# Kernel optimization log

Hardware: AMD Instinct MI355X
Metric: run time of the kernel (lower is better)

Reference implementation:

```python
import jax, jax.numpy as jnp
import numpy as np

PAD = 0          # pad_token_id == blank_index in the source module
NEG = -1e30      # log-space 'zero' (safe for fp32)


def _ctc_mean_loss(labels, logits, logits_mask):
    """Faithful jnp port of CTCLoss.call: tf.nn.ctc_loss (alpha forward DP,
    blank=pad, dense labels, logits [B,T,V]) + feasibility mask + mean."""
    B, T, V = logits.shape
    L = labels.shape[1]
    S = 2 * L + 1

    labels_len = jnp.sum(labels != PAD, axis=-1).astype(jnp.int32)   # [B]
    logits_len = jnp.sum(logits_mask, axis=-1).astype(jnp.int32)     # [B]

    logp = jax.nn.log_softmax(logits.astype(jnp.float32), axis=-1)   # [B,T,V]

    # Blank-interleaved extended label sequence: (blank, l1, blank, l2, ..., blank)
    ext = jnp.full((B, S), PAD, dtype=labels.dtype)
    ext = ext.at[:, 1::2].set(labels)                                # [B,S]
    ext_m2 = jnp.pad(ext, ((0, 0), (2, 0)), constant_values=PAD)[:, :S]
    allow_skip = (ext != PAD) & (ext != ext_m2)                      # [B,S]

    # Emission log-probs gathered at extended labels: em[b,t,s] = logp[b,t,ext[b,s]]
    em = jnp.take_along_axis(logp, jnp.broadcast_to(ext[:, None, :], (B, T, S)), axis=2)
    em = em.transpose(1, 0, 2)                                       # [T,B,S]

    neg = jnp.float32(NEG)
    alpha0 = jnp.full((B, S), neg, dtype=jnp.float32)
    alpha0 = alpha0.at[:, 0].set(em[0, :, 0]).at[:, 1].set(em[0, :, 1])

    t_idx = jnp.arange(1, T, dtype=jnp.int32)
    active = t_idx[:, None] < logits_len[None, :]                    # [T-1,B]

    def step(alpha, inp):
        em_t, act = inp                                              # [B,S], [B]
        p1 = jnp.concatenate([jnp.full((B, 1), neg), alpha[:, :-1]], axis=1)
        p2 = jnp.concatenate([jnp.full((B, 2), neg), alpha[:, :-2]], axis=1)
        p2 = jnp.where(allow_skip, p2, neg)
        new = em_t + jnp.logaddexp(jnp.logaddexp(alpha, p1), p2)
        alpha = jnp.where(act[:, None], new, alpha)                  # freeze past logit_len
        return alpha, None

    alpha, _ = jax.lax.scan(step, alpha0, (em[1:], active))          # [B,S]

    e = 2 * labels_len                                               # end of extended seq
    a_end = jnp.take_along_axis(alpha, e[:, None], axis=1)[:, 0]
    a_end1 = jnp.take_along_axis(alpha, jnp.maximum(e - 1, 0)[:, None], axis=1)[:, 0]
    loss = -jnp.logaddexp(a_end, a_end1)                             # per-example NLL

    loss_mask = (labels_len <= logits_len).astype(jnp.float32)
    return jnp.mean(loss * loss_mask)


def setup_inputs() -> dict:
    key = jax.random.key(0)
    k1, k2, k3, k4 = jax.random.split(key, 4)
    B, T, V, L = 256, 1024, 64, 64

    lab_len = jax.random.randint(k1, (B,), L // 2, L + 1)            # [32,64]
    vals = jax.random.randint(k2, (B, L), 1, V)                      # non-blank tokens
    labels = jnp.where(jnp.arange(L)[None, :] < lab_len[:, None], vals, 0).astype(jnp.int64)

    log_len = jax.random.randint(k3, (B,), 2 * L + 64, T + 1)        # feasible alignments
    logits_mask = jnp.arange(T)[None, :] < log_len[:, None]          # prefix-True mask

    logits = jax.random.normal(k4, (B, T, V), dtype=jnp.float32)
    return {"labels": labels, "logits": logits, "logits_mask": logits_mask}


def reference(labels, logits, logits_mask):
    return _ctc_mean_loss(labels, logits, logits_mask)
```

## Files before the change

### kernel.cpp

```cpp
#include <hip/hip_runtime.h>

#define BB 256
#define TT 1024
#define VV 64
#define LL 64
#define LOG2E 1.4426950408889634f
#define LN2   0.6931471805599453f

__device__ __forceinline__ int   f2i(float x) { return __float_as_int(x); }
__device__ __forceinline__ float i2f(int x)   { return __int_as_float(x); }

__device__ __forceinline__ float wave_max63(float x) {
  x = fmaxf(x, i2f(__builtin_amdgcn_update_dpp(0, f2i(x), 0x111, 0xF, 0xF, true)));
  x = fmaxf(x, i2f(__builtin_amdgcn_update_dpp(0, f2i(x), 0x112, 0xF, 0xF, true)));
  x = fmaxf(x, i2f(__builtin_amdgcn_update_dpp(0, f2i(x), 0x114, 0xF, 0xF, true)));
  x = fmaxf(x, i2f(__builtin_amdgcn_update_dpp(0, f2i(x), 0x118, 0xF, 0xF, true)));
  x = fmaxf(x, i2f(__builtin_amdgcn_update_dpp(0, f2i(x), 0x142, 0xF, 0xF, true)));
  x = fmaxf(x, i2f(__builtin_amdgcn_update_dpp(0, f2i(x), 0x143, 0xF, 0xF, true)));
  return i2f(__builtin_amdgcn_readlane(f2i(x), 63));
}

extern "C" __global__ void __launch_bounds__(384, 1)
ctc_fused(const int* __restrict__ labels, const float* __restrict__ logits,
          const int* __restrict__ mask, float* __restrict__ out) {
  __shared__ float lsePart[4];
  __shared__ float sG0v[64], sG1v[64];
  __shared__ float sG2s;
  __shared__ int   sCtB;
  const int b = blockIdx.x;
  const int tid = threadIdx.x;
  const int lane = tid & 63;
  const int wv = tid >> 6;

  const float* lg = logits + (size_t)b * TT * VV;

  int lsum = 0;
  const int* mrow = mask + b * TT;
#pragma unroll
  for (int k = 0; k < TT / 64; ++k) lsum += mrow[lane + (k << 6)];
#pragma unroll
  for (int off = 32; off; off >>= 1) lsum += __shfl_xor(lsum, off);
  int len = __builtin_amdgcn_readfirstlane(lsum);
  len = len < 1 ? 1 : (len > TT ? TT : len);
  const int nwin = (len + 15) >> 4;
  int mid = len >> 1; mid = mid < 1 ? 1 : mid;
  const int nwF = (mid + 15) >> 4;
  const int nwB = (len - mid + 15) >> 4;

  int lab_len = 0;
  float A0 = 0.0f, A1 = 0.0f, A2 = 0.0f;
  int ctotA = 0;

#define RENORM3(X, Y, Z, CT) { \
    const float mxv = wave_max63(fmaxf(fmaxf(X, Y), Z)); \
    const int eb_ = (f2i(mxv) >> 23) & 255; \
    int kk = (eb_ > 0 && eb_ < 255) ? (187 - eb_) : 0; \
    kk = kk > 126 ? 126 : (kk < -126 ? -126 : kk); \
    CT += kk; \
    const float sc = i2f((127 + kk) << 23); \
    X *= sc; Y *= sc; Z *= sc; \
  }

#define RESCALE45(X, Y, Z, CT) { \
    const float mxv = wave_max63(fmaxf(fmaxf(X, Y), Z)); \
    const int eb_ = (f2i(mxv) >> 23) & 255; \
    int kk = (eb_ > 0 && eb_ < 255) ? (172 - eb_) : 0; \
    kk = kk > 126 ? 126 : (kk < -126 ? -126 : kk); \
    CT += kk; \
    const float sc = i2f((127 + kk) << 23); \
    X *= sc; Y *= sc; Z *= sc; \
  }

  if (wv == 0) {
    const int lab = labels[b * LL + lane] & 63;
    lab_len = (int)__popcll(__ballot(lab != 0));
    const int plab = __builtin_amdgcn_update_dpp(0, lab, 0x138, 0xF, 0xF, false);
    const float sk = (lab != 0 && lab != plab) ? 1.0f : 0.0f;
    A0 = (lane == 0) ? 1.0f : 0.0f;
    __builtin_amdgcn_s_setprio(1);

    const int cu = lane & 15;
    const float* lgg = lg + lab;
    const float* lgc = lg + (cu << 6);

    float qa_c, qb_c, qc_c;
    float qa_g0, qa_g1, qa_g2, qa_g3, qa_g4, qa_g5, qa_g6, qa_g7,
          qa_g8, qa_g9, qa_g10, qa_g11, qa_g12, qa_g13, qa_g14, qa_g15;
    float qb_g0, qb_g1, qb_g2, qb_g3, qb_g4, qb_g5, qb_g6, qb_g7,
          qb_g8, qb_g9, qb_g10, qb_g11, qb_g12, qb_g13, qb_g14, qb_g15;
    float qc_g0, qc_g1, qc_g2, qc_g3, qc_g4, qc_g5, qc_g6, qc_g7,
          qc_g8, qc_g9, qc_g10, qc_g11, qc_g12, qc_g13, qc_g14, qc_g15;

#define FISSUE(WN, S) { \
    const float* pg_ = lgg + ((WN) << 10); \
    S##_g0  = pg_[0];    S##_g1  = pg_[64];   S##_g2  = pg_[128];  S##_g3  = pg_[192]; \
    S##_g4  = pg_[256];  S##_g5  = pg_[320];  S##_g6  = pg_[384];  S##_g7  = pg_[448]; \
    S##_g8  = pg_[512];  S##_g9  = pg_[576];  S##_g10 = pg_[640];  S##_g11 = pg_[704]; \
    S##_g12 = pg_[768];  S##_g13 = pg_[832];  S##_g14 = pg_[896];  S##_g15 = pg_[960]; \
    S##_c = lgc[(WN) << 10]; \
  }

#define FSTEPU(U) { \
    const float A1p = i2f(__builtin_amdgcn_update_dpp(0, f2i(A1), 0x138, 0xF, 0xF, false)); \
    const float nA0 = c##U * (A0 + A1p); \
    const float nA1 = g##U * fmaf(sk, A1p, A0 + A1); \
    A2 = c##U * (A2 + A1); \
    A0 = nA0; A1 = nA1; \
  }

#define FSTEPM(U) { \
    const float A1p = i2f(__builtin_amdgcn_update_dpp(0, f2i(A1), 0x138, 0xF, 0xF, false)); \
    const float nA0 = c##U * (A0 + A1p); \
    const float nA1 = g##U * fmaf(sk, A1p, A0 + A1); \
    const float nA2 = c##U * (A2 + A1); \
    const bool act = (tbase + (U)) < mid; \
    A0 = act ? nA0 : A0; A1 = act ? nA1 : A1; A2 = act ? nA2 : A2; \
  }

#define FBODY(W, S) { \
    const float cv = __builtin_amdgcn_exp2f(S##_c * LOG2E); \
    const float g0  = __builtin_amdgcn_exp2f(S##_g0  * LOG2E); \
    const float g1  = __builtin_amdgcn_exp2f(S##_g1  * LOG2E); \
    const float g2  = __builtin_amdgcn_exp2f(S##_g2  * LOG2E); \
    const float g3  = __builtin_amdgcn_exp2f(S##_g3  * LOG2E); \
    const float g4  = __builtin_amdgcn_exp2f(S##_g4  * LOG2E); \
    const float g5  = __builtin_amdgcn_exp2f(S##_g5  * LOG2E); \
    const float g6  = __builtin_amdgcn_exp2f(S##_g6  * LOG2E); \
    const float g7  = __builtin_amdgcn_exp2f(S##_g7  * LOG2E); \
    const float g8  = __builtin_amdgcn_exp2f(S##_g8  * LOG2E); \
    const float g9  = __builtin_amdgcn_exp2f(S##_g9  * LOG2E); \
    const float g10 = __builtin_amdgcn_exp2f(S##_g10 * LOG2E); \
    const float g11 = __builtin_amdgcn_exp2f(S##_g11 * LOG2E); \
    const float g12 = __builtin_amdgcn_exp2f(S##_g12 * LOG2E); \
    const float g13 = __builtin_amdgcn_exp2f(S##_g13 * LOG2E); \
    const float g14 = __builtin_amdgcn_exp2f(S##_g14 * LOG2E); \
    const float g15 = __builtin_amdgcn_exp2f(S##_g15 * LOG2E); \
    if ((W) + 3 < 64) { FISSUE((W) + 3, S) } \
    const float c0  = i2f(__builtin_amdgcn_readlane(f2i(cv), 0)); \
    const float c1  = i2f(__builtin_amdgcn_readlane(f2i(cv), 1)); \
    const float c2  = i2f(__builtin_amdgcn_readlane(f2i(cv), 2)); \
    const float c3  = i2f(__builtin_amdgcn_readlane(f2i(cv), 3)); \
    const float c4  = i2f(__builtin_amdgcn_readlane(f2i(cv), 4)); \
    const float c5  = i2f(__builtin_amdgcn_readlane(f2i(cv), 5)); \
    const float c6  = i2f(__builtin_amdgcn_readlane(f2i(cv), 6)); \
    const float c7  = i2f(__builtin_amdgcn_readlane(f2i(cv), 7)); \
    const float c8  = i2f(__builtin_amdgcn_readlane(f2i(cv), 8)); \
    const float c9  = i2f(__builtin_amdgcn_readlane(f2i(cv), 9)); \
    const float c10 = i2f(__builtin_amdgcn_readlane(f2i(cv), 10)); \
    const float c11 = i2f(__builtin_amdgcn_readlane(f2i(cv), 11)); \
    const float c12 = i2f(__builtin_amdgcn_readlane(f2i(cv), 12)); \
    const float c13 = i2f(__builtin_amdgcn_readlane(f2i(cv), 13)); \
    const float c14 = i2f(__builtin_amdgcn_readlane(f2i(cv), 14)); \
    const float c15 = i2f(__builtin_amdgcn_readlane(f2i(cv), 15)); \
    RENORM3(A0, A1, A2, ctotA) \
    const int tbase = (W) << 4; \
    if (tbase + 16 <= mid) { \
      FSTEPU(0)  FSTEPU(1)  FSTEPU(2)  FSTEPU(3)  FSTEPU(4)  FSTEPU(5)  FSTEPU(6)  FSTEPU(7) \
      FSTEPU(8)  FSTEPU(9)  FSTEPU(10) FSTEPU(11) FSTEPU(12) FSTEPU(13) FSTEPU(14) FSTEPU(15) \
    } else { \
      FSTEPM(0)  FSTEPM(1)  FSTEPM(2)  FSTEPM(3)  FSTEPM(4)  FSTEPM(5)  FSTEPM(6)  FSTEPM(7) \
      FSTEPM(8)  FSTEPM(9)  FSTEPM(10) FSTEPM(11) FSTEPM(12) FSTEPM(13) FSTEPM(14) FSTEPM(15) \
    } \
  }

    FISSUE(0, qa) FISSUE(1, qb) FISSUE(2, qc)
    int w = 0;
    for (; w + 3 <= nwF; w += 3) {
      FBODY(w, qa) FBODY(w + 1, qb) FBODY(w + 2, qc)
    }
    if (w < nwF) { FBODY(w, qa) ++w; }
    if (w < nwF) { FBODY(w, qb) ++w; }
#undef FBODY
#undef FSTEPM
#undef FSTEPU
#undef FISSUE
    RESCALE45(A0, A1, A2, ctotA)

  } else if (wv == 1) {
    const int lab = labels[b * LL + lane] & 63;
    const int ll = (int)__popcll(__ballot(lab != 0));
    const int plab = __builtin_amdgcn_update_dpp(0, lab, 0x138, 0xF, 0xF, false);
    const float sk = (lab != 0 && lab != plab) ? 1.0f : 0.0f;
    const float skp = i2f(__builtin_amdgcn_update_dpp(0, f2i(sk), 0x130, 0xF, 0xF, false));
    const bool is63 = (lane == 63);
    __builtin_amdgcn_s_setprio(1);

    float G0 = 0.0f, G1 = 0.0f, G2 = 0.0f;
    if (ll == 0)            { G0 = (lane == 0) ? 2.0f : 0.0f; }
    else if (ll >= LL)      { G2 = 1.0f; G1 = is63 ? 1.0f : 0.0f; }
    else {
      G0 = (lane == ll) ? 1.0f : 0.0f;
      G1 = (lane == ll - 1) ? 1.0f : 0.0f;
    }
    int ctotB = 0;

    const int cu = lane & 15;
    const float* lgg = lg + lab;

    float ra_c, rb_c, rc_c;
    float ra_g0, ra_g1, ra_g2, ra_g3, ra_g4, ra_g5, ra_g6, ra_g7,
          ra_g8, ra_g9, ra_g10, ra_g11, ra_g12, ra_g13, ra_g14, ra_g15;
    float rb_g0, rb_g1, rb_g2, rb_g3, rb_g4, rb_g5, rb_g6, rb_g7,
          rb_g8, rb_g9, rb_g10, rb_g11, rb_g12, rb_g13, rb_g14, rb_g15;
    float rc_g0, rc_g1, rc_g2, rc_g3, rc_g4, rc_g5, rc_g6, rc_g7,
          rc_g8, rc_g9, rc_g10, rc_g11, rc_g12, rc_g13, rc_g14, rc_g15;

#define BLD(RW) ( (RW) < 0 ? 0 : (RW) )
#define BISSUE(J, S) { \
    const int br_ = len - 1 - ((J) << 4); \
    S##_g0  = lgg[BLD(br_ - 0)  << 6]; S##_g1  = lgg[BLD(br_ - 1)  << 6]; \
    S##_g2  = lgg[BLD(br_ - 2)  << 6]; S##_g3  = lgg[BLD(br_ - 3)  << 6]; \
    S##_g4  = lgg[BLD(br_ - 4)  << 6]; S##_g5  = lgg[BLD(br_ - 5)  << 6]; \
    S##_g6  = lgg[BLD(br_ - 6)  << 6]; S##_g7  = lgg[BLD(br_ - 7)  << 6]; \
    S##_g8  = lgg[BLD(br_ - 8)  << 6]; S##_g9  = lgg[BLD(br_ - 9)  << 6]; \
    S##_g10 = lgg[BLD(br_ - 10) << 6]; S##_g11 = lgg[BLD(br_ - 11) << 6]; \
    S##_g12 = lgg[BLD(br_ - 12) << 6]; S##_g13 = lgg[BLD(br_ - 13) << 6]; \
    S##_g14 = lgg[BLD(br_ - 14) << 6]; S##_g15 = lgg[BLD(br_ - 15) << 6]; \
    S##_c = lg[BLD(br_ - cu) << 6]; \
  }

#define BSTEPU(U) { \
    const float V_ = i2f(__builtin_amdgcn_update_dpp(0, f2i(G1), 0x130, 0xF, 0xF, false)); \
    float U_ = i2f(__builtin_amdgcn_update_dpp(0, f2i(G0), 0x130, 0xF, 0xF, false)); \
    U_ = is63 ? G2 : U_; \
    const float nG0 = fmaf(cB##U, G0, gB##U * G1); \
    const float nG1 = fmaf(gB##U, G1, fmaf(cB##U, U_, hB##U * V_)); \
    G2 = cB##U * G2; \
    G0 = nG0; G1 = nG1; \
  }

#define BSTEPM(U) { \
    const float V_ = i2f(__builtin_amdgcn_update_dpp(0, f2i(G1), 0x130, 0xF, 0xF, false)); \
    float U_ = i2f(__builtin_amdgcn_update_dpp(0, f2i(G0), 0x130, 0xF, 0xF, false)); \
    U_ = is63 ? G2 : U_; \
    const float nG0 = fmaf(cB##U, G0, gB##U * G1); \
    const float nG1 = fmaf(gB##U, G1, fmaf(cB##U, U_, hB##U * V_)); \
    const float nG2 = cB##U * G2; \
    const bool act = (brow0 - (U)) >= mid; \
    G0 = act ? nG0 : G0; G1 = act ? nG1 : G1; G2 = act ? nG2 : G2; \
  }

#define BPREP(U, S) \
    const float gB##U = __builtin_amdgcn_exp2f(S##_g##U * LOG2E); \
    const float hB##U = skp * i2f(__builtin_amdgcn_update_dpp(0, f2i(gB##U), 0x130, 0xF, 0xF, false));

#define BBODY(J, S) { \
    const int brow0 = len - 1 - ((J) << 4); \
    const float cv = __builtin_amdgcn_exp2f(S##_c * LOG2E); \
    BPREP(0, S)  BPREP(1, S)  BPREP(2, S)  BPREP(3, S) \
    BPREP(4, S)  BPREP(5, S)  BPREP(6, S)  BPREP(7, S) \
    BPREP(8, S)  BPREP(9, S)  BPREP(10, S) BPREP(11, S) \
    BPREP(12, S) BPREP(13, S) BPREP(14, S) BPREP(15, S) \
    if ((J) + 3 < 64) { BISSUE((J) + 3, S) } \
    const float cB0  = i2f(__builtin_amdgcn_readlane(f2i(cv), 0)); \
    const float cB1  = i2f(__builtin_amdgcn_readlane(f2i(cv), 1)); \
    const float cB2  = i2f(__builtin_amdgcn_readlane(f2i(cv), 2)); \
    const float cB3  = i2f(__builtin_amdgcn_readlane(f2i(cv), 3)); \
    const float cB4  = i2f(__builtin_amdgcn_readlane(f2i(cv), 4)); \
    const float cB5  = i2f(__builtin_amdgcn_readlane(f2i(cv), 5)); \
    const float cB6  = i2f(__builtin_amdgcn_readlane(f2i(cv), 6)); \
    const float cB7  = i2f(__builtin_amdgcn_readlane(f2i(cv), 7)); \
    const float cB8  = i2f(__builtin_amdgcn_readlane(f2i(cv), 8)); \
    const float cB9  = i2f(__builtin_amdgcn_readlane(f2i(cv), 9)); \
    const float cB10 = i2f(__builtin_amdgcn_readlane(f2i(cv), 10)); \
    const float cB11 = i2f(__builtin_amdgcn_readlane(f2i(cv), 11)); \
    const float cB12 = i2f(__builtin_amdgcn_readlane(f2i(cv), 12)); \
    const float cB13 = i2f(__builtin_amdgcn_readlane(f2i(cv), 13)); \
    const float cB14 = i2f(__builtin_amdgcn_readlane(f2i(cv), 14)); \
    const float cB15 = i2f(__builtin_amdgcn_readlane(f2i(cv), 15)); \
    RENORM3(G0, G1, G2, ctotB) \
    if (brow0 - 15 >= mid) { \
      BSTEPU(0)  BSTEPU(1)  BSTEPU(2)  BSTEPU(3)  BSTEPU(4)  BSTEPU(5)  BSTEPU(6)  BSTEPU(7) \
      BSTEPU(8)  BSTEPU(9)  BSTEPU(10) BSTEPU(11) BSTEPU(12) BSTEPU(13) BSTEPU(14) BSTEPU(15) \
    } else { \
      BSTEPM(0)  BSTEPM(1)  BSTEPM(2)  BSTEPM(3)  BSTEPM(4)  BSTEPM(5)  BSTEPM(6)  BSTEPM(7) \
      BSTEPM(8)  BSTEPM(9)  BSTEPM(10) BSTEPM(11) BSTEPM(12) BSTEPM(13) BSTEPM(14) BSTEPM(15) \
    } \
  }

    BISSUE(0, ra) BISSUE(1, rb) BISSUE(2, rc)
    int j = 0;
    for (; j + 3 <= nwB; j += 3) {
      BBODY(j, ra) BBODY(j + 1, rb) BBODY(j + 2, rc)
    }
    if (j < nwB) { BBODY(j, ra) ++j; }
    if (j < nwB) { BBODY(j, rb) ++j; }
#undef BBODY
#undef BPREP
#undef BSTEPM
#undef BSTEPU
#undef BISSUE
#undef BLD
    RESCALE45(G0, G1, G2, ctotB)

    sG0v[lane] = G0;
    sG1v[lane] = G1;
    if (is63) sG2s = G2;
    if (lane == 0) sCtB = ctotB;

  } else {
    const int pw = wv - 2;
    const int prow = lane >> 4;
    const int pcol = (lane & 15) << 2;
    const float* pb_ = lg + ((((pw << 2) + prow) << 6) + pcol);
    float acc = 0.0f;
    float4 pa, pb, pc;

#define LISSUE(K, S) { S = *(const float4*)(pb_ + ((K) << 10)); }

#define LBODY(K, S) { \
    const float e0 = __builtin_amdgcn_exp2f(S.x * LOG2E); \
    const float e1 = __builtin_amdgcn_exp2f(S.y * LOG2E); \
    const float e2 = __builtin_amdgcn_exp2f(S.z * LOG2E); \
    const float e3 = __builtin_amdgcn_exp2f(S.w * LOG2E); \
    if ((K) + 3 < 64) { LISSUE((K) + 3, S) } \
    float s = (e0 + e1) + (e2 + e3); \
    s += i2f(__builtin_amdgcn_update_dpp(0, f2i(s), 0x111, 0xF, 0xF, true)); \
    s += i2f(__builtin_amdgcn_update_dpp(0, f2i(s), 0x112, 0xF, 0xF, true)); \
    s += i2f(__builtin_amdgcn_update_dpp(0, f2i(s), 0x114, 0xF, 0xF, true)); \
    s += i2f(__builtin_amdgcn_update_dpp(0, f2i(s), 0x118, 0xF, 0xF, true)); \
    if ((lane & 15) == 15 && ((((K) << 4) + (pw << 2) + prow) < len)) acc += __logf(s); \
  }

    LISSUE(0, pa) LISSUE(1, pb) LISSUE(2, pc)
    int k = 0;
    for (; k + 3 <= nwin; k += 3) {
      LBODY(k, pa) LBODY(k + 1, pb) LBODY(k + 2, pc)
    }
    if (k < nwin) { LBODY(k, pa) ++k; }
    if (k < nwin) { LBODY(k, pb) ++k; }
#undef LBODY
#undef LISSUE

    float a = ((lane & 15) == 15) ? acc : 0.0f;
    a += __shfl_xor(a, 16);
    a += __shfl_xor(a, 32);
    if (lane == 63) lsePart[pw] = a;
  }

  __syncthreads();

  if (wv == 0) {
    float prod = A0 * sG0v[lane] + A1 * sG1v[lane];
    if (lane == 63) prod = fmaf(A2, sG2s, prod);
#pragma unroll
    for (int off = 32; off; off >>= 1) prod += __shfl_xor(prod, off);
    const float p = fmaxf(prod, 1e-37f);
    float loss = ((lsePart[0] + lsePart[1]) + (lsePart[2] + lsePart[3]))
               - LN2 * (__builtin_amdgcn_logf(p) - (float)(ctotA + sCtB));
    if (lab_len > len) loss = 0.0f;
    if (lane == 0) atomicAdd(out, loss * (1.0f / 256.0f));
  }
#undef RESCALE45
#undef RENORM3
}

extern "C" void kernel_launch(void* const* d_in, const int* in_sizes, int n_in,
                              void* d_out, int out_size, void* d_ws, size_t ws_size,
                              hipStream_t stream) {
  (void)in_sizes; (void)n_in; (void)out_size; (void)d_ws; (void)ws_size;
  hipMemsetAsync(d_out, 0, sizeof(float), stream);
  ctc_fused<<<dim3(BB), dim3(384), 0, stream>>>(
      (const int*)d_in[0], (const float*)d_in[1], (const int*)d_in[2], (float*)d_out);
}
```

Baseline: 119.6 us.

## Split logsumexp waves into forward/backward halves with deeper load prefetch

The four logsumexp waves are regrouped so two walk the forward half of the time axis and two walk the backward half in reverse. This follows the same order as the forward and backward alpha/beta DP waves, so the logits rows they touch are likely still in cache. Each wave now handles two rows per step and keeps eight steps of float4 loads in flight instead of three, which hides more memory latency. The cost is many more live registers and clamped out-of-range loads in padded tail iterations.

```diff
diff --git a/kernel.cpp b/kernel.cpp
--- a/kernel.cpp
+++ b/kernel.cpp
@@ -42,7 +42,6 @@
   for (int off = 32; off; off >>= 1) lsum += __shfl_xor(lsum, off);
   int len = __builtin_amdgcn_readfirstlane(lsum);
   len = len < 1 ? 1 : (len > TT ? TT : len);
-  const int nwin = (len + 15) >> 4;
   int mid = len >> 1; mid = mid < 1 ? 1 : mid;
   const int nwF = (mid + 15) >> 4;
   const int nwB = (len - mid + 15) >> 4;
@@ -299,43 +298,91 @@
     if (lane == 0) sCtB = ctotB;
 
   } else {
-    const int pw = wv - 2;
-    const int prow = lane >> 4;
-    const int pcol = (lane & 15) << 2;
-    const float* pb_ = lg + ((((pw << 2) + prow) << 6) + pcol);
+    const int q = lane >> 4;
+    const int u15 = ((lane & 15) == 15);
+    const int colv2 = (lane & 15) << 2;
+    const int TTm1 = TT - 1;
     float acc = 0.0f;
-    float4 pa, pb, pc;
-
-#define LISSUE(K, S) { S = *(const float4*)(pb_ + ((K) << 10)); }
-
-#define LBODY(K, S) { \
-    const float e0 = __builtin_amdgcn_exp2f(S.x * LOG2E); \
-    const float e1 = __builtin_amdgcn_exp2f(S.y * LOG2E); \
-    const float e2 = __builtin_amdgcn_exp2f(S.z * LOG2E); \
-    const float e3 = __builtin_amdgcn_exp2f(S.w * LOG2E); \
-    if ((K) + 3 < 64) { LISSUE((K) + 3, S) } \
-    float s = (e0 + e1) + (e2 + e3); \
-    s += i2f(__builtin_amdgcn_update_dpp(0, f2i(s), 0x111, 0xF, 0xF, true)); \
-    s += i2f(__builtin_amdgcn_update_dpp(0, f2i(s), 0x112, 0xF, 0xF, true)); \
-    s += i2f(__builtin_amdgcn_update_dpp(0, f2i(s), 0x114, 0xF, 0xF, true)); \
-    s += i2f(__builtin_amdgcn_update_dpp(0, f2i(s), 0x118, 0xF, 0xF, true)); \
-    if ((lane & 15) == 15 && ((((K) << 4) + (pw << 2) + prow) < len)) acc += __logf(s); \
-  }
-
-    LISSUE(0, pa) LISSUE(1, pb) LISSUE(2, pc)
-    int k = 0;
-    for (; k + 3 <= nwin; k += 3) {
-      LBODY(k, pa) LBODY(k + 1, pb) LBODY(k + 2, pc)
-    }
-    if (k < nwin) { LBODY(k, pa) ++k; }
-    if (k < nwin) { LBODY(k, pb) ++k; }
-#undef LBODY
-#undef LISSUE
-
-    float a = ((lane & 15) == 15) ? acc : 0.0f;
+    float4 e0A, e0B, e1A, e1B, e2A, e2B, e3A, e3B,
+           e4A, e4B, e5A, e5B, e6A, e6B, e7A, e7B;
+
+#define LSUM(V, S) \
+    float S = (__builtin_amdgcn_exp2f((V).x * LOG2E) + __builtin_amdgcn_exp2f((V).y * LOG2E)) \
+            + (__builtin_amdgcn_exp2f((V).z * LOG2E) + __builtin_amdgcn_exp2f((V).w * LOG2E)); \
+    S += i2f(__builtin_amdgcn_update_dpp(0, f2i(S), 0x111, 0xF, 0xF, true)); \
+    S += i2f(__builtin_amdgcn_update_dpp(0, f2i(S), 0x112, 0xF, 0xF, true)); \
+    S += i2f(__builtin_amdgcn_update_dpp(0, f2i(S), 0x114, 0xF, 0xF, true)); \
+    S += i2f(__builtin_amdgcn_update_dpp(0, f2i(S), 0x118, 0xF, 0xF, true));
+
+    if (wv < 4) {
+      const int f = wv - 2;
+#define LFISSUE(K, SA, SB) { \
+      int rA_ = ((K) << 4) + (f << 3) + q; \
+      int rB_ = rA_ + 4; \
+      rA_ = rA_ > TTm1 ? TTm1 : rA_; \
+      rB_ = rB_ > TTm1 ? TTm1 : rB_; \
+      SA = *(const float4*)(lg + (rA_ << 6) + colv2); \
+      SB = *(const float4*)(lg + (rB_ << 6) + colv2); \
+    }
+#define LFBODY(K, SA, SB) { \
+      const int rA_ = ((K) << 4) + (f << 3) + q; \
+      const float4 vA_ = SA, vB_ = SB; \
+      LFISSUE((K) + 8, SA, SB) \
+      LSUM(vA_, sA_) \
+      LSUM(vB_, sB_) \
+      if (u15 && rA_ < mid) acc += __logf(sA_); \
+      if (u15 && rA_ + 4 < mid) acc += __logf(sB_); \
+    }
+      const int nwl = (mid + 15) >> 4;
+      const int NB8 = ((nwl + 7) >> 3) << 3;
+      LFISSUE(0, e0A, e0B) LFISSUE(1, e1A, e1B) LFISSUE(2, e2A, e2B) LFISSUE(3, e3A, e3B)
+      LFISSUE(4, e4A, e4B) LFISSUE(5, e5A, e5B) LFISSUE(6, e6A, e6B) LFISSUE(7, e7A, e7B)
+      for (int k = 0; k < NB8; k += 8) {
+        LFBODY(k + 0, e0A, e0B) LFBODY(k + 1, e1A, e1B)
+        LFBODY(k + 2, e2A, e2B) LFBODY(k + 3, e3A, e3B)
+        LFBODY(k + 4, e4A, e4B) LFBODY(k + 5, e5A, e5B)
+        LFBODY(k + 6, e6A, e6B) LFBODY(k + 7, e7A, e7B)
+      }
+#undef LFBODY
+#undef LFISSUE
+    } else {
+      const int bw = wv - 4;
+#define LBISSUE(J, SA, SB) { \
+      int rA_ = len - 1 - ((J) << 4) - (bw << 3) - q; \
+      int rB_ = rA_ - 4; \
+      rA_ = rA_ < 0 ? 0 : rA_; \
+      rB_ = rB_ < 0 ? 0 : rB_; \
+      SA = *(const float4*)(lg + (rA_ << 6) + colv2); \
+      SB = *(const float4*)(lg + (rB_ << 6) + colv2); \
+    }
+#define LBBODY(J, SA, SB) { \
+      const int rA_ = len - 1 - ((J) << 4) - (bw << 3) - q; \
+      const float4 vA_ = SA, vB_ = SB; \
+      LBISSUE((J) + 8, SA, SB) \
+      LSUM(vA_, sA_) \
+      LSUM(vB_, sB_) \
+      if (u15 && rA_ >= mid) acc += __logf(sA_); \
+      if (u15 && rA_ - 4 >= mid) acc += __logf(sB_); \
+    }
+      const int nwl = (len - mid + 15) >> 4;
+      const int NB8 = ((nwl + 7) >> 3) << 3;
+      LBISSUE(0, e0A, e0B) LBISSUE(1, e1A, e1B) LBISSUE(2, e2A, e2B) LBISSUE(3, e3A, e3B)
+      LBISSUE(4, e4A, e4B) LBISSUE(5, e5A, e5B) LBISSUE(6, e6A, e6B) LBISSUE(7, e7A, e7B)
+      for (int j = 0; j < NB8; j += 8) {
+        LBBODY(j + 0, e0A, e0B) LBBODY(j + 1, e1A, e1B)
+        LBBODY(j + 2, e2A, e2B) LBBODY(j + 3, e3A, e3B)
+        LBBODY(j + 4, e4A, e4B) LBBODY(j + 5, e5A, e5B)
+        LBBODY(j + 6, e6A, e6B) LBBODY(j + 7, e7A, e7B)
+      }
+#undef LBBODY
+#undef LBISSUE
+    }
+#undef LSUM
+
+    float a = u15 ? acc : 0.0f;
     a += __shfl_xor(a, 16);
     a += __shfl_xor(a, 32);
-    if (lane == 63) lsePart[pw] = a;
+    if (lane == 63) lsePart[wv - 2] = a;
   }
 
   __syncthreads();
```

Result: no change. 120.6 us (+0.9%).

## Split log-sum-exp into a separate wide kernel ahead of the DP kernel

Applied to the files above, without the earlier changes.

Moves the per-timestep log-sum-exp reduction out of the fused 384-thread kernel into its own kernel launched over 2048 blocks, which writes partial sums to the workspace. The DP kernel now runs only the forward and backward waves with 128 threads and reads the partial sums back. The aim is to stop the LSE waves from contending with the latency-bound DP waves on the same CU, and to spread the LSE work across the whole GPU. The cost is an extra kernel launch, a workspace round trip, and LSE no longer overlapping with the DP.

```diff
diff --git a/kernel.cpp b/kernel.cpp
--- a/kernel.cpp
+++ b/kernel.cpp
@@ -20,10 +20,46 @@
   return i2f(__builtin_amdgcn_readlane(f2i(x), 63));
 }
 
-extern "C" __global__ void __launch_bounds__(384, 1)
-ctc_fused(const int* __restrict__ labels, const float* __restrict__ logits,
-          const int* __restrict__ mask, float* __restrict__ out) {
-  __shared__ float lsePart[4];
+extern "C" __global__ void __launch_bounds__(256, 4)
+ctc_lse(const float* __restrict__ logits, const int* __restrict__ mask,
+        float* __restrict__ ws) {
+  const int blk = blockIdx.x;
+  const int b = blk >> 3, seg = blk & 7;
+  const int tid = threadIdx.x, lane = tid & 63, wv = tid >> 6;
+  const float* lg = logits + (size_t)b * TT * VV;
+  const int* mrow = mask + b * TT;
+  const int q = lane >> 4, colv = (lane & 15) << 2;
+  const int r0 = (seg << 7) + (wv << 5) + q;
+
+#define AL(I) \
+  const float4 v##I = *(const float4*)(lg + ((r0 + ((I) << 2)) << 6) + colv); \
+  const int    m##I = mrow[r0 + ((I) << 2)];
+  AL(0) AL(1) AL(2) AL(3) AL(4) AL(5) AL(6) AL(7)
+#undef AL
+
+  float acc = 0.0f;
+#define AB(I) { \
+    float s = (__builtin_amdgcn_exp2f(v##I.x * LOG2E) + __builtin_amdgcn_exp2f(v##I.y * LOG2E)) \
+            + (__builtin_amdgcn_exp2f(v##I.z * LOG2E) + __builtin_amdgcn_exp2f(v##I.w * LOG2E)); \
+    s += i2f(__builtin_amdgcn_update_dpp(0, f2i(s), 0x111, 0xF, 0xF, true)); \
+    s += i2f(__builtin_amdgcn_update_dpp(0, f2i(s), 0x112, 0xF, 0xF, true)); \
+    s += i2f(__builtin_amdgcn_update_dpp(0, f2i(s), 0x114, 0xF, 0xF, true)); \
+    s += i2f(__builtin_amdgcn_update_dpp(0, f2i(s), 0x118, 0xF, 0xF, true)); \
+    if ((lane & 15) == 15 && m##I) acc += __logf(s); \
+  }
+  AB(0) AB(1) AB(2) AB(3) AB(4) AB(5) AB(6) AB(7)
+#undef AB
+
+  float a = ((lane & 15) == 15) ? acc : 0.0f;
+  a += __shfl_xor(a, 16);
+  a += __shfl_xor(a, 32);
+  if (lane == 63) ws[(b << 5) + (seg << 2) + wv] = a;
+}
+
+extern "C" __global__ void __launch_bounds__(128, 1)
+ctc_dp(const int* __restrict__ labels, const float* __restrict__ logits,
+       const int* __restrict__ mask, const float* __restrict__ ws,
+       float* __restrict__ out) {
   __shared__ float sG0v[64], sG1v[64];
   __shared__ float sG2s;
   __shared__ int   sCtB;
@@ -42,7 +78,6 @@
   for (int off = 32; off; off >>= 1) lsum += __shfl_xor(lsum, off);
   int len = __builtin_amdgcn_readfirstlane(lsum);
   len = len < 1 ? 1 : (len > TT ? TT : len);
-  const int nwin = (len + 15) >> 4;
   int mid = len >> 1; mid = mid < 1 ? 1 : mid;
   const int nwF = (mid + 15) >> 4;
   const int nwB = (len - mid + 15) >> 4;
@@ -176,7 +211,7 @@
 #undef FISSUE
     RESCALE45(A0, A1, A2, ctotA)
 
-  } else if (wv == 1) {
+  } else {
     const int lab = labels[b * LL + lane] & 63;
     const int ll = (int)__popcll(__ballot(lab != 0));
     const int plab = __builtin_amdgcn_update_dpp(0, lab, 0x138, 0xF, 0xF, false);
@@ -297,45 +332,6 @@
     sG1v[lane] = G1;
     if (is63) sG2s = G2;
     if (lane == 0) sCtB = ctotB;
-
-  } else {
-    const int pw = wv - 2;
-    const int prow = lane >> 4;
-    const int pcol = (lane & 15) << 2;
-    const float* pb_ = lg + ((((pw << 2) + prow) << 6) + pcol);
-    float acc = 0.0f;
-    float4 pa, pb, pc;
-
-#define LISSUE(K, S) { S = *(const float4*)(pb_ + ((K) << 10)); }
-
-#define LBODY(K, S) { \
-    const float e0 = __builtin_amdgcn_exp2f(S.x * LOG2E); \
-    const float e1 = __builtin_amdgcn_exp2f(S.y * LOG2E); \
-    const float e2 = __builtin_amdgcn_exp2f(S.z * LOG2E); \
-    const float e3 = __builtin_amdgcn_exp2f(S.w * LOG2E); \
-    if ((K) + 3 < 64) { LISSUE((K) + 3, S) } \
-    float s = (e0 + e1) + (e2 + e3); \
-    s += i2f(__builtin_amdgcn_update_dpp(0, f2i(s), 0x111, 0xF, 0xF, true)); \
-    s += i2f(__builtin_amdgcn_update_dpp(0, f2i(s), 0x112, 0xF, 0xF, true)); \
-    s += i2f(__builtin_amdgcn_update_dpp(0, f2i(s), 0x114, 0xF, 0xF, true)); \
-    s += i2f(__builtin_amdgcn_update_dpp(0, f2i(s), 0x118, 0xF, 0xF, true)); \
-    if ((lane & 15) == 15 && ((((K) << 4) + (pw << 2) + prow) < len)) acc += __logf(s); \
-  }
-
-    LISSUE(0, pa) LISSUE(1, pb) LISSUE(2, pc)
-    int k = 0;
-    for (; k + 3 <= nwin; k += 3) {
-      LBODY(k, pa) LBODY(k + 1, pb) LBODY(k + 2, pc)
-    }
-    if (k < nwin) { LBODY(k, pa) ++k; }
-    if (k < nwin) { LBODY(k, pb) ++k; }
-#undef LBODY
-#undef LISSUE
-
-    float a = ((lane & 15) == 15) ? acc : 0.0f;
-    a += __shfl_xor(a, 16);
-    a += __shfl_xor(a, 32);
-    if (lane == 63) lsePart[pw] = a;
   }
 
   __syncthreads();
@@ -346,9 +342,17 @@
 #pragma unroll
     for (int off = 32; off; off >>= 1) prod += __shfl_xor(prod, off);
     const float p = fmaxf(prod, 1e-37f);
-    float loss = ((lsePart[0] + lsePart[1]) + (lsePart[2] + lsePart[3]))
-               - LN2 * (__builtin_amdgcn_logf(p) - (float)(ctotA + sCtB));
-    if (lab_len > len) loss = 0.0f;
+
+    float lse = (lane < 32) ? ws[(b << 5) + lane] : 0.0f;
+    lse += __shfl_xor(lse, 1);
+    lse += __shfl_xor(lse, 2);
+    lse += __shfl_xor(lse, 4);
+    lse += __shfl_xor(lse, 8);
+    lse += __shfl_xor(lse, 16);
+
+    float loss = lse - LN2 * (__builtin_amdgcn_logf(p) - (float)(ctotA + sCtB));
+    int ll0 = lab_len;
+    if (ll0 > len) loss = 0.0f;
     if (lane == 0) atomicAdd(out, loss * (1.0f / 256.0f));
   }
 #undef RESCALE45
@@ -358,8 +362,11 @@
 extern "C" void kernel_launch(void* const* d_in, const int* in_sizes, int n_in,
                               void* d_out, int out_size, void* d_ws, size_t ws_size,
                               hipStream_t stream) {
-  (void)in_sizes; (void)n_in; (void)out_size; (void)d_ws; (void)ws_size;
+  (void)in_sizes; (void)n_in; (void)out_size; (void)ws_size;
   hipMemsetAsync(d_out, 0, sizeof(float), stream);
-  ctc_fused<<<dim3(BB), dim3(384), 0, stream>>>(
-      (const int*)d_in[0], (const float*)d_in[1], (const int*)d_in[2], (float*)d_out);
+  ctc_lse<<<dim3(BB * 8), dim3(256), 0, stream>>>(
+      (const float*)d_in[1], (const int*)d_in[2], (float*)d_ws);
+  ctc_dp<<<dim3(BB), dim3(128), 0, stream>>>(
+      (const int*)d_in[0], (const float*)d_in[1], (const int*)d_in[2],
+      (const float*)d_ws, (float*)d_out);
 }
```

After: 125.0 us. +4.5%, slower.

## Stage emission gathers into LDS via direct global-to-LDS loads

Applied to the files above, without the earlier changes.

Replaces the register-held triple-buffered global loads in the forward and backward DP waves with global_load_lds DMA into a four-slot LDS ring, waited on with explicit vmcnt counters. The per-lane blank-column values are now read from LDS as float4 and exponentiated per element, instead of one exp per lane followed by 16 readlane broadcasts. This is meant to cut VGPR pressure and cross-lane readlane cost on the serial critical path. In exchange it adds LDS read latency, 16 extra exp ops per step, and relies on hand-tuned vmcnt accounting, which could cause stalls or races if the count is wrong. The loads for w+3 are also issued past the end of the loop range without bounds checks.

```diff
diff --git a/kernel.cpp b/kernel.cpp
--- a/kernel.cpp
+++ b/kernel.cpp
@@ -20,9 +20,19 @@
   return i2f(__builtin_amdgcn_readlane(f2i(x), 63));
 }
 
+__device__ __forceinline__ void gload4(const float* g, float* l) {
+  __builtin_amdgcn_global_load_lds(
+      (const __attribute__((address_space(1))) unsigned int*)g,
+      (__attribute__((address_space(3))) unsigned int*)l, 4, 0, 0);
+}
+
 extern "C" __global__ void __launch_bounds__(384, 1)
 ctc_fused(const int* __restrict__ labels, const float* __restrict__ logits,
           const int* __restrict__ mask, float* __restrict__ out) {
+  __shared__ __align__(16) float gFl[4][16][64];
+  __shared__ __align__(16) float cFl[4][64];
+  __shared__ __align__(16) float gBl[4][16][64];
+  __shared__ __align__(16) float cBl[4][64];
   __shared__ float lsePart[4];
   __shared__ float sG0v[64], sG1v[64];
   __shared__ float sG2s;
@@ -81,23 +91,26 @@
 
     const int cu = lane & 15;
     const float* lgg = lg + lab;
-    const float* lgc = lg + (cu << 6);
-
-    float qa_c, qb_c, qc_c;
-    float qa_g0, qa_g1, qa_g2, qa_g3, qa_g4, qa_g5, qa_g6, qa_g7,
-          qa_g8, qa_g9, qa_g10, qa_g11, qa_g12, qa_g13, qa_g14, qa_g15;
-    float qb_g0, qb_g1, qb_g2, qb_g3, qb_g4, qb_g5, qb_g6, qb_g7,
-          qb_g8, qb_g9, qb_g10, qb_g11, qb_g12, qb_g13, qb_g14, qb_g15;
-    float qc_g0, qc_g1, qc_g2, qc_g3, qc_g4, qc_g5, qc_g6, qc_g7,
-          qc_g8, qc_g9, qc_g10, qc_g11, qc_g12, qc_g13, qc_g14, qc_g15;
-
-#define FISSUE(WN, S) { \
-    const float* pg_ = lgg + ((WN) << 10); \
-    S##_g0  = pg_[0];    S##_g1  = pg_[64];   S##_g2  = pg_[128];  S##_g3  = pg_[192]; \
-    S##_g4  = pg_[256];  S##_g5  = pg_[320];  S##_g6  = pg_[384];  S##_g7  = pg_[448]; \
-    S##_g8  = pg_[512];  S##_g9  = pg_[576];  S##_g10 = pg_[640];  S##_g11 = pg_[704]; \
-    S##_g12 = pg_[768];  S##_g13 = pg_[832];  S##_g14 = pg_[896];  S##_g15 = pg_[960]; \
-    S##_c = lgc[(WN) << 10]; \
+
+#define FDMA(WN) { \
+    const int rw_ = (WN) << 4; const int sl_ = (WN) & 3; \
+    gload4(lgg + ((rw_ + 0)  << 6), &gFl[sl_][0][0]);  \
+    gload4(lgg + ((rw_ + 1)  << 6), &gFl[sl_][1][0]);  \
+    gload4(lgg + ((rw_ + 2)  << 6), &gFl[sl_][2][0]);  \
+    gload4(lgg + ((rw_ + 3)  << 6), &gFl[sl_][3][0]);  \
+    gload4(lgg + ((rw_ + 4)  << 6), &gFl[sl_][4][0]);  \
+    gload4(lgg + ((rw_ + 5)  << 6), &gFl[sl_][5][0]);  \
+    gload4(lgg + ((rw_ + 6)  << 6), &gFl[sl_][6][0]);  \
+    gload4(lgg + ((rw_ + 7)  << 6), &gFl[sl_][7][0]);  \
+    gload4(lgg + ((rw_ + 8)  << 6), &gFl[sl_][8][0]);  \
+    gload4(lgg + ((rw_ + 9)  << 6), &gFl[sl_][9][0]);  \
+    gload4(lgg + ((rw_ + 10) << 6), &gFl[sl_][10][0]); \
+    gload4(lgg + ((rw_ + 11) << 6), &gFl[sl_][11][0]); \
+    gload4(lgg + ((rw_ + 12) << 6), &gFl[sl_][12][0]); \
+    gload4(lgg + ((rw_ + 13) << 6), &gFl[sl_][13][0]); \
+    gload4(lgg + ((rw_ + 14) << 6), &gFl[sl_][14][0]); \
+    gload4(lgg + ((rw_ + 15) << 6), &gFl[sl_][15][0]); \
+    gload4(lg + ((rw_ + cu) << 6),  &cFl[sl_][0]);     \
   }
 
 #define FSTEPU(U) { \
@@ -117,64 +130,60 @@
     A0 = act ? nA0 : A0; A1 = act ? nA1 : A1; A2 = act ? nA2 : A2; \
   }
 
-#define FBODY(W, S) { \
-    const float cv = __builtin_amdgcn_exp2f(S##_c * LOG2E); \
-    const float g0  = __builtin_amdgcn_exp2f(S##_g0  * LOG2E); \
-    const float g1  = __builtin_amdgcn_exp2f(S##_g1  * LOG2E); \
-    const float g2  = __builtin_amdgcn_exp2f(S##_g2  * LOG2E); \
-    const float g3  = __builtin_amdgcn_exp2f(S##_g3  * LOG2E); \
-    const float g4  = __builtin_amdgcn_exp2f(S##_g4  * LOG2E); \
-    const float g5  = __builtin_amdgcn_exp2f(S##_g5  * LOG2E); \
-    const float g6  = __builtin_amdgcn_exp2f(S##_g6  * LOG2E); \
-    const float g7  = __builtin_amdgcn_exp2f(S##_g7  * LOG2E); \
-    const float g8  = __builtin_amdgcn_exp2f(S##_g8  * LOG2E); \
-    const float g9  = __builtin_amdgcn_exp2f(S##_g9  * LOG2E); \
-    const float g10 = __builtin_amdgcn_exp2f(S##_g10 * LOG2E); \
-    const float g11 = __builtin_amdgcn_exp2f(S##_g11 * LOG2E); \
-    const float g12 = __builtin_amdgcn_exp2f(S##_g12 * LOG2E); \
-    const float g13 = __builtin_amdgcn_exp2f(S##_g13 * LOG2E); \
-    const float g14 = __builtin_amdgcn_exp2f(S##_g14 * LOG2E); \
-    const float g15 = __builtin_amdgcn_exp2f(S##_g15 * LOG2E); \
-    if ((W) + 3 < 64) { FISSUE((W) + 3, S) } \
-    const float c0  = i2f(__builtin_amdgcn_readlane(f2i(cv), 0)); \
-    const float c1  = i2f(__builtin_amdgcn_readlane(f2i(cv), 1)); \
-    const float c2  = i2f(__builtin_amdgcn_readlane(f2i(cv), 2)); \
-    const float c3  = i2f(__builtin_amdgcn_readlane(f2i(cv), 3)); \
-    const float c4  = i2f(__builtin_amdgcn_readlane(f2i(cv), 4)); \
-    const float c5  = i2f(__builtin_amdgcn_readlane(f2i(cv), 5)); \
-    const float c6  = i2f(__builtin_amdgcn_readlane(f2i(cv), 6)); \
-    const float c7  = i2f(__builtin_amdgcn_readlane(f2i(cv), 7)); \
-    const float c8  = i2f(__builtin_amdgcn_readlane(f2i(cv), 8)); \
-    const float c9  = i2f(__builtin_amdgcn_readlane(f2i(cv), 9)); \
-    const float c10 = i2f(__builtin_amdgcn_readlane(f2i(cv), 10)); \
-    const float c11 = i2f(__builtin_amdgcn_readlane(f2i(cv), 11)); \
-    const float c12 = i2f(__builtin_amdgcn_readlane(f2i(cv), 12)); \
-    const float c13 = i2f(__builtin_amdgcn_readlane(f2i(cv), 13)); \
-    const float c14 = i2f(__builtin_amdgcn_readlane(f2i(cv), 14)); \
-    const float c15 = i2f(__builtin_amdgcn_readlane(f2i(cv), 15)); \
-    RENORM3(A0, A1, A2, ctotA) \
-    const int tbase = (W) << 4; \
-    if (tbase + 16 <= mid) { \
-      FSTEPU(0)  FSTEPU(1)  FSTEPU(2)  FSTEPU(3)  FSTEPU(4)  FSTEPU(5)  FSTEPU(6)  FSTEPU(7) \
-      FSTEPU(8)  FSTEPU(9)  FSTEPU(10) FSTEPU(11) FSTEPU(12) FSTEPU(13) FSTEPU(14) FSTEPU(15) \
-    } else { \
-      FSTEPM(0)  FSTEPM(1)  FSTEPM(2)  FSTEPM(3)  FSTEPM(4)  FSTEPM(5)  FSTEPM(6)  FSTEPM(7) \
-      FSTEPM(8)  FSTEPM(9)  FSTEPM(10) FSTEPM(11) FSTEPM(12) FSTEPM(13) FSTEPM(14) FSTEPM(15) \
-    } \
-  }
-
-    FISSUE(0, qa) FISSUE(1, qb) FISSUE(2, qc)
-    int w = 0;
-    for (; w + 3 <= nwF; w += 3) {
-      FBODY(w, qa) FBODY(w + 1, qb) FBODY(w + 2, qc)
+    FDMA(0) FDMA(1) FDMA(2)
+
+    for (int w = 0; w < nwF; ++w) {
+      asm volatile("s_waitcnt vmcnt(34)");
+      __builtin_amdgcn_sched_barrier(0);
+      FDMA(w + 3)
+      const int sl = w & 3;
+      const float* gr = &gFl[sl][0][0] + lane;
+      float g0  = gr[0],    g1  = gr[64],   g2  = gr[128],  g3  = gr[192],
+            g4  = gr[256],  g5  = gr[320],  g6  = gr[384],  g7  = gr[448],
+            g8  = gr[512],  g9  = gr[576],  g10 = gr[640],  g11 = gr[704],
+            g12 = gr[768],  g13 = gr[832],  g14 = gr[896],  g15 = gr[960];
+      const float4* cp = (const float4*)&cFl[sl][0];
+      const float4 ca = cp[0], cb = cp[1], cc = cp[2], cd = cp[3];
+      g0  = __builtin_amdgcn_exp2f(g0  * LOG2E); g1  = __builtin_amdgcn_exp2f(g1  * LOG2E);
+      g2  = __builtin_amdgcn_exp2f(g2  * LOG2E); g3  = __builtin_amdgcn_exp2f(g3  * LOG2E);
+      g4  = __builtin_amdgcn_exp2f(g4  * LOG2E); g5  = __builtin_amdgcn_exp2f(g5  * LOG2E);
+      g6  = __builtin_amdgcn_exp2f(g6  * LOG2E); g7  = __builtin_amdgcn_exp2f(g7  * LOG2E);
+      g8  = __builtin_amdgcn_exp2f(g8  * LOG2E); g9  = __builtin_amdgcn_exp2f(g9  * LOG2E);
+      g10 = __builtin_amdgcn_exp2f(g10 * LOG2E); g11 = __builtin_amdgcn_exp2f(g11 * LOG2E);
+      g12 = __builtin_amdgcn_exp2f(g12 * LOG2E); g13 = __builtin_amdgcn_exp2f(g13 * LOG2E);
+      g14 = __builtin_amdgcn_exp2f(g14 * LOG2E); g15 = __builtin_amdgcn_exp2f(g15 * LOG2E);
+      const float c0  = __builtin_amdgcn_exp2f(ca.x * LOG2E);
+      const float c1  = __builtin_amdgcn_exp2f(ca.y * LOG2E);
+      const float c2  = __builtin_amdgcn_exp2f(ca.z * LOG2E);
+      const float c3  = __builtin_amdgcn_exp2f(ca.w * LOG2E);
+      const float c4  = __builtin_amdgcn_exp2f(cb.x * LOG2E);
+      const float c5  = __builtin_amdgcn_exp2f(cb.y * LOG2E);
+      const float c6  = __builtin_amdgcn_exp2f(cb.z * LOG2E);
+      const float c7  = __builtin_amdgcn_exp2f(cb.w * LOG2E);
+      const float c8  = __builtin_amdgcn_exp2f(cc.x * LOG2E);
+      const float c9  = __builtin_amdgcn_exp2f(cc.y * LOG2E);
+      const float c10 = __builtin_amdgcn_exp2f(cc.z * LOG2E);
+      const float c11 = __builtin_amdgcn_exp2f(cc.w * LOG2E);
+      const float c12 = __builtin_amdgcn_exp2f(cd.x * LOG2E);
+      const float c13 = __builtin_amdgcn_exp2f(cd.y * LOG2E);
+      const float c14 = __builtin_amdgcn_exp2f(cd.z * LOG2E);
+      const float c15 = __builtin_amdgcn_exp2f(cd.w * LOG2E);
+      RENORM3(A0, A1, A2, ctotA)
+      const int tbase = w << 4;
+      if (tbase + 16 <= mid) {
+        FSTEPU(0)  FSTEPU(1)  FSTEPU(2)  FSTEPU(3)  FSTEPU(4)  FSTEPU(5)  FSTEPU(6)  FSTEPU(7)
+        FSTEPU(8)  FSTEPU(9)  FSTEPU(10) FSTEPU(11) FSTEPU(12) FSTEPU(13) FSTEPU(14) FSTEPU(15)
+      } else {
+        FSTEPM(0)  FSTEPM(1)  FSTEPM(2)  FSTEPM(3)  FSTEPM(4)  FSTEPM(5)  FSTEPM(6)  FSTEPM(7)
+        FSTEPM(8)  FSTEPM(9)  FSTEPM(10) FSTEPM(11) FSTEPM(12) FSTEPM(13) FSTEPM(14) FSTEPM(15)
+      }
     }
-    if (w < nwF) { FBODY(w, qa) ++w; }
-    if (w < nwF) { FBODY(w, qb) ++w; }
-#undef FBODY
+    asm volatile("s_waitcnt vmcnt(0)");
+    __builtin_amdgcn_sched_barrier(0);
+    RESCALE45(A0, A1, A2, ctotA)
 #undef FSTEPM
 #undef FSTEPU
-#undef FISSUE
-    RESCALE45(A0, A1, A2, ctotA)
+#undef FDMA
 
   } else if (wv == 1) {
     const int lab = labels[b * LL + lane] & 63;
@@ -197,26 +206,26 @@
     const int cu = lane & 15;
     const float* lgg = lg + lab;
 
-    float ra_c, rb_c, rc_c;
-    float ra_g0, ra_g1, ra_g2, ra_g3, ra_g4, ra_g5, ra_g6, ra_g7,
-          ra_g8, ra_g9, ra_g10, ra_g11, ra_g12, ra_g13, ra_g14, ra_g15;
-    float rb_g0, rb_g1, rb_g2, rb_g3, rb_g4, rb_g5, rb_g6, rb_g7,
-          rb_g8, rb_g9, rb_g10, rb_g11, rb_g12, rb_g13, rb_g14, rb_g15;
-    float rc_g0, rc_g1, rc_g2, rc_g3, rc_g4, rc_g5, rc_g6, rc_g7,
-          rc_g8, rc_g9, rc_g10, rc_g11, rc_g12, rc_g13, rc_g14, rc_g15;
-
 #define BLD(RW) ( (RW) < 0 ? 0 : (RW) )
-#define BISSUE(J, S) { \
-    const int br_ = len - 1 - ((J) << 4); \
-    S##_g0  = lgg[BLD(br_ - 0)  << 6]; S##_g1  = lgg[BLD(br_ - 1)  << 6]; \
-    S##_g2  = lgg[BLD(br_ - 2)  << 6]; S##_g3  = lgg[BLD(br_ - 3)  << 6]; \
-    S##_g4  = lgg[BLD(br_ - 4)  << 6]; S##_g5  = lgg[BLD(br_ - 5)  << 6]; \
-    S##_g6  = lgg[BLD(br_ - 6)  << 6]; S##_g7  = lgg[BLD(br_ - 7)  << 6]; \
-    S##_g8  = lgg[BLD(br_ - 8)  << 6]; S##_g9  = lgg[BLD(br_ - 9)  << 6]; \
-    S##_g10 = lgg[BLD(br_ - 10) << 6]; S##_g11 = lgg[BLD(br_ - 11) << 6]; \
-    S##_g12 = lgg[BLD(br_ - 12) << 6]; S##_g13 = lgg[BLD(br_ - 13) << 6]; \
-    S##_g14 = lgg[BLD(br_ - 14) << 6]; S##_g15 = lgg[BLD(br_ - 15) << 6]; \
-    S##_c = lg[BLD(br_ - cu) << 6]; \
+#define BDMA(JN) { \
+    const int br_ = len - 1 - ((JN) << 4); const int sl_ = (JN) & 3; \
+    gload4(lgg + (BLD(br_ - 0)  << 6), &gBl[sl_][0][0]);  \
+    gload4(lgg + (BLD(br_ - 1)  << 6), &gBl[sl_][1][0]);  \
+    gload4(lgg + (BLD(br_ - 2)  << 6), &gBl[sl_][2][0]);  \
+    gload4(lgg + (BLD(br_ - 3)  << 6), &gBl[sl_][3][0]);  \
+    gload4(lgg + (BLD(br_ - 4)  << 6), &gBl[sl_][4][0]);  \
+    gload4(lgg + (BLD(br_ - 5)  << 6), &gBl[sl_][5][0]);  \
+    gload4(lgg + (BLD(br_ - 6)  << 6), &gBl[sl_][6][0]);  \
+    gload4(lgg + (BLD(br_ - 7)  << 6), &gBl[sl_][7][0]);  \
+    gload4(lgg + (BLD(br_ - 8)  << 6), &gBl[sl_][8][0]);  \
+    gload4(lgg + (BLD(br_ - 9)  << 6), &gBl[sl_][9][0]);  \
+    gload4(lgg + (BLD(br_ - 10) << 6), &gBl[sl_][10][0]); \
+    gload4(lgg + (BLD(br_ - 11) << 6), &gBl[sl_][11][0]); \
+    gload4(lgg + (BLD(br_ - 12) << 6), &gBl[sl_][12][0]); \
+    gload4(lgg + (BLD(br_ - 13) << 6), &gBl[sl_][13][0]); \
+    gload4(lgg + (BLD(br_ - 14) << 6), &gBl[sl_][14][0]); \
+    gload4(lgg + (BLD(br_ - 15) << 6), &gBl[sl_][15][0]); \
+    gload4(lg + (BLD(br_ - cu) << 6),  &cBl[sl_][0]);     \
   }
 
 #define BSTEPU(U) { \
@@ -240,58 +249,60 @@
     G0 = act ? nG0 : G0; G1 = act ? nG1 : G1; G2 = act ? nG2 : G2; \
   }
 
-#define BPREP(U, S) \
-    const float gB##U = __builtin_amdgcn_exp2f(S##_g##U * LOG2E); \
+#define BPREP(U) \
+    const float gB##U = __builtin_amdgcn_exp2f(r##U * LOG2E); \
     const float hB##U = skp * i2f(__builtin_amdgcn_update_dpp(0, f2i(gB##U), 0x130, 0xF, 0xF, false));
 
-#define BBODY(J, S) { \
-    const int brow0 = len - 1 - ((J) << 4); \
-    const float cv = __builtin_amdgcn_exp2f(S##_c * LOG2E); \
-    BPREP(0, S)  BPREP(1, S)  BPREP(2, S)  BPREP(3, S) \
-    BPREP(4, S)  BPREP(5, S)  BPREP(6, S)  BPREP(7, S) \
-    BPREP(8, S)  BPREP(9, S)  BPREP(10, S) BPREP(11, S) \
-    BPREP(12, S) BPREP(13, S) BPREP(14, S) BPREP(15, S) \
-    if ((J) + 3 < 64) { BISSUE((J) + 3, S) } \
-    const float cB0  = i2f(__builtin_amdgcn_readlane(f2i(cv), 0)); \
-    const float cB1  = i2f(__builtin_amdgcn_readlane(f2i(cv), 1)); \
-    const float cB2  = i2f(__builtin_amdgcn_readlane(f2i(cv), 2)); \
-    const float cB3  = i2f(__builtin_amdgcn_readlane(f2i(cv), 3)); \
-    const float cB4  = i2f(__builtin_amdgcn_readlane(f2i(cv), 4)); \
-    const float cB5  = i2f(__builtin_amdgcn_readlane(f2i(cv), 5)); \
-    const float cB6  = i2f(__builtin_amdgcn_readlane(f2i(cv), 6)); \
-    const float cB7  = i2f(__builtin_amdgcn_readlane(f2i(cv), 7)); \
-    const float cB8  = i2f(__builtin_amdgcn_readlane(f2i(cv), 8)); \
-    const float cB9  = i2f(__builtin_amdgcn_readlane(f2i(cv), 9)); \
-    const float cB10 = i2f(__builtin_amdgcn_readlane(f2i(cv), 10)); \
-    const float cB11 = i2f(__builtin_amdgcn_readlane(f2i(cv), 11)); \
-    const float cB12 = i2f(__builtin_amdgcn_readlane(f2i(cv), 12)); \
-    const float cB13 = i2f(__builtin_amdgcn_readlane(f2i(cv), 13)); \
-    const float cB14 = i2f(__builtin_amdgcn_readlane(f2i(cv), 14)); \
-    const float cB15 = i2f(__builtin_amdgcn_readlane(f2i(cv), 15)); \
-    RENORM3(G0, G1, G2, ctotB) \
-    if (brow0 - 15 >= mid) { \
-      BSTEPU(0)  BSTEPU(1)  BSTEPU(2)  BSTEPU(3)  BSTEPU(4)  BSTEPU(5)  BSTEPU(6)  BSTEPU(7) \
-      BSTEPU(8)  BSTEPU(9)  BSTEPU(10) BSTEPU(11) BSTEPU(12) BSTEPU(13) BSTEPU(14) BSTEPU(15) \
-    } else { \
-      BSTEPM(0)  BSTEPM(1)  BSTEPM(2)  BSTEPM(3)  BSTEPM(4)  BSTEPM(5)  BSTEPM(6)  BSTEPM(7) \
-      BSTEPM(8)  BSTEPM(9)  BSTEPM(10) BSTEPM(11) BSTEPM(12) BSTEPM(13) BSTEPM(14) BSTEPM(15) \
-    } \
-  }
-
-    BISSUE(0, ra) BISSUE(1, rb) BISSUE(2, rc)
-    int j = 0;
-    for (; j + 3 <= nwB; j += 3) {
-      BBODY(j, ra) BBODY(j + 1, rb) BBODY(j + 2, rc)
+    BDMA(0) BDMA(1) BDMA(2)
+
+    for (int j = 0; j < nwB; ++j) {
+      asm volatile("s_waitcnt vmcnt(34)");
+      __builtin_amdgcn_sched_barrier(0);
+      BDMA(j + 3)
+      const int sl = j & 3;
+      const int brow0 = len - 1 - (j << 4);
+      const float* gr = &gBl[sl][0][0] + lane;
+      const float r0  = gr[0],    r1  = gr[64],   r2  = gr[128],  r3  = gr[192],
+                  r4  = gr[256],  r5  = gr[320],  r6  = gr[384],  r7  = gr[448],
+                  r8  = gr[512],  r9  = gr[576],  r10 = gr[640],  r11 = gr[704],
+                  r12 = gr[768],  r13 = gr[832],  r14 = gr[896],  r15 = gr[960];
+      const float4* cp = (const float4*)&cBl[sl][0];
+      const float4 ca = cp[0], cb = cp[1], cc = cp[2], cd = cp[3];
+      BPREP(0)  BPREP(1)  BPREP(2)  BPREP(3)  BPREP(4)  BPREP(5)  BPREP(6)  BPREP(7)
+      BPREP(8)  BPREP(9)  BPREP(10) BPREP(11) BPREP(12) BPREP(13) BPREP(14) BPREP(15)
+      const float cB0  = __builtin_amdgcn_exp2f(ca.x * LOG2E);
+      const float cB1  = __builtin_amdgcn_exp2f(ca.y * LOG2E);
+      const float cB2  = __builtin_amdgcn_exp2f(ca.z * LOG2E);
+      const float cB3  = __builtin_amdgcn_exp2f(ca.w * LOG2E);
+      const float cB4  = __builtin_amdgcn_exp2f(cb.x * LOG2E);
+      const float cB5  = __builtin_amdgcn_exp2f(cb.y * LOG2E);
+      const float cB6  = __builtin_amdgcn_exp2f(cb.z * LOG2E);
+      const float cB7  = __builtin_amdgcn_exp2f(cb.w * LOG2E);
+      const float cB8  = __builtin_amdgcn_exp2f(cc.x * LOG2E);
+      const float cB9  = __builtin_amdgcn_exp2f(cc.y * LOG2E);
+      const float cB10 = __builtin_amdgcn_exp2f(cc.z * LOG2E);
+      const float cB11 = __builtin_amdgcn_exp2f(cc.w * LOG2E);
+      const float cB12 = __builtin_amdgcn_exp2f(cd.x * LOG2E);
+      const float cB13 = __builtin_amdgcn_exp2f(cd.y * LOG2E);
+      const float cB14 = __builtin_amdgcn_exp2f(cd.z * LOG2E);
+      const float cB15 = __builtin_amdgcn_exp2f(cd.w * LOG2E);
+      RENORM3(G0, G1, G2, ctotB)
+      if (brow0 - 15 >= mid) {
+        BSTEPU(0)  BSTEPU(1)  BSTEPU(2)  BSTEPU(3)  BSTEPU(4)  BSTEPU(5)  BSTEPU(6)  BSTEPU(7)
+        BSTEPU(8)  BSTEPU(9)  BSTEPU(10) BSTEPU(11) BSTEPU(12) BSTEPU(13) BSTEPU(14) BSTEPU(15)
+      } else {
+        BSTEPM(0)  BSTEPM(1)  BSTEPM(2)  BSTEPM(3)  BSTEPM(4)  BSTEPM(5)  BSTEPM(6)  BSTEPM(7)
+        BSTEPM(8)  BSTEPM(9)  BSTEPM(10) BSTEPM(11) BSTEPM(12) BSTEPM(13) BSTEPM(14) BSTEPM(15)
+      }
     }
-    if (j < nwB) { BBODY(j, ra) ++j; }
-    if (j < nwB) { BBODY(j, rb) ++j; }
-#undef BBODY
+    asm volatile("s_waitcnt vmcnt(0)");
+    __builtin_amdgcn_sched_barrier(0);
+    RESCALE45(G0, G1, G2, ctotB)
 #undef BPREP
 #undef BSTEPM
 #undef BSTEPU
-#undef BISSUE
+#undef BDMA
 #undef BLD
-    RESCALE45(G0, G1, G2, ctotB)
 
     sG0v[lane] = G0;
     sG1v[lane] = G1;
```

Measured after the change: 129.1 us. 7.9% more time.
